# Kernel tuning notes

Hardware: AMD Instinct MI355X
Metric: run time of the kernel (lower is better)

The kernel has to match this reference:

```python
import jax, jax.numpy as jnp
import numpy as np

EMBED_DIM = 1024
NUM_HEADS = 16
HEAD_DIM = EMBED_DIM // NUM_HEADS


def setup_inputs() -> dict:
    key = jax.random.key(0)
    k_h, k_q, k_k, k_v, k_o = jax.random.split(key, 5)
    scale = 1.0 / np.sqrt(EMBED_DIM)
    return {
        "h": jax.random.normal(k_h, (2, 2048, EMBED_DIM), dtype=jnp.float32),
        "W_q": jax.random.normal(k_q, (EMBED_DIM, EMBED_DIM), dtype=jnp.float32) * scale,
        "W_k": jax.random.normal(k_k, (EMBED_DIM, EMBED_DIM), dtype=jnp.float32) * scale,
        "W_v": jax.random.normal(k_v, (EMBED_DIM, EMBED_DIM), dtype=jnp.float32) * scale,
        "W_o": jax.random.normal(k_o, (EMBED_DIM, EMBED_DIM), dtype=jnp.float32) * scale,
    }


def reference(h, W_q, W_k, W_v, W_o):
    B, S, E = h.shape
    H, D = NUM_HEADS, HEAD_DIM
    # nn.Linear stores weight as [out, in]; y = x @ W.T
    q = (h @ W_q.T).reshape(B, S, H, D).transpose(0, 2, 1, 3)  # [B,H,S,D]
    k = (h @ W_k.T).reshape(B, S, H, D).transpose(0, 2, 1, 3)
    v = (h @ W_v.T).reshape(B, S, H, D).transpose(0, 2, 1, 3)
    scores = jnp.einsum("bhsd,bhtd->bhst", q, k) / np.sqrt(D)
    attn = jax.nn.softmax(scores, axis=-1)
    ctx = jnp.einsum("bhst,bhtd->bhsd", attn, v)  # [B,H,S,D]
    ctx = ctx.transpose(0, 2, 1, 3).reshape(B, S, E)
    return ctx @ W_o.T
```

## Files before the change

### kernel.cpp

```cpp
#include <hip/hip_runtime.h>
#include <hip/hip_bf16.h>

#define B_ 2
#define S_ 2048
#define E_ 1024
#define H_ 16
#define D_ 64
#define M_ (B_*S_)

typedef __attribute__((ext_vector_type(8))) short bf16x8;
typedef __attribute__((ext_vector_type(4))) float f32x4;
typedef __attribute__((ext_vector_type(8))) unsigned short u16x8;
typedef __attribute__((ext_vector_type(4))) unsigned short u16x4;

__device__ __forceinline__ unsigned short f2bf_hw(float f) {
  union { __hip_bfloat16 h; unsigned short u; } c;
  c.h = __float2bfloat16(f);
  return c.u;
}

__device__ __forceinline__ void gload_lds16(const void* g, void* l) {
  __builtin_amdgcn_global_load_lds(
      (const __attribute__((address_space(1))) void*)g,
      (__attribute__((address_space(3))) void*)l, 16, 0, 0);
}

__global__ __launch_bounds__(256) void cvt_all(const float* __restrict__ h,
                                               const float* __restrict__ Wq,
                                               const float* __restrict__ Wk,
                                               const float* __restrict__ Wv,
                                               const float* __restrict__ Wo,
                                               unsigned short* __restrict__ dst,
                                               float qscale) {
  int i = blockIdx.x * 256 + threadIdx.x;
  const float4* src4;
  int idx;
  float scale = 1.f;
  if (i < (1 << 20)) {
    src4 = (const float4*)h; idx = i;
  } else {
    int t = i - (1 << 20);
    int j = t >> 18;
    idx = t & ((1 << 18) - 1);
    src4 = (const float4*)((j == 0) ? Wq : (j == 1) ? Wk : (j == 2) ? Wv : Wo);
    if (j == 0) scale = qscale;
  }
  float4 v = src4[idx];
  u16x4 o;
  o[0] = f2bf_hw(v.x * scale);
  o[1] = f2bf_hw(v.y * scale);
  o[2] = f2bf_hw(v.z * scale);
  o[3] = f2bf_hw(v.w * scale);
  ((u16x4*)dst)[i] = o;
}

template<int OUT_BF16>
__device__ __forceinline__ void gemm_body(const unsigned short* __restrict__ A,
                                          const unsigned short* __restrict__ W,
                                          void* __restrict__ Cv,
                                          int row0, int col0, int N, int K,
                                          unsigned short* As, unsigned short* Bs) {
  const int tid = threadIdx.x;
  const int lane = tid & 63, wave = tid >> 6;
  const int wr = wave >> 1, wc = wave & 1;
  const int lq = lane & 15, lg = lane >> 4;
  f32x4 acc[4][4] = {};

  for (int kt = 0; kt < K; kt += 32) {
#pragma unroll
    for (int i = 0; i < 2; ++i) {
      int t = tid + i * 256;
      int rr = t >> 2;
      int sch = (t & 3) ^ ((rr >> 1) & 3);
      gload_lds16(A + (size_t)(row0 + rr) * K + kt + sch * 8, &As[t * 8]);
      gload_lds16(W + (size_t)(col0 + rr) * K + kt + sch * 8, &Bs[t * 8]);
    }
    __syncthreads();
    bf16x8 af[4], bfr[4];
#pragma unroll
    for (int mi = 0; mi < 4; ++mi) {
      int row = wr * 64 + mi * 16 + lq;
      af[mi] = *(const bf16x8*)&As[row * 32 + (lg ^ ((row >> 1) & 3)) * 8];
    }
#pragma unroll
    for (int ni = 0; ni < 4; ++ni) {
      int row = wc * 64 + ni * 16 + lq;
      bfr[ni] = *(const bf16x8*)&Bs[row * 32 + (lg ^ ((row >> 1) & 3)) * 8];
    }
#pragma unroll
    for (int mi = 0; mi < 4; ++mi)
#pragma unroll
      for (int ni = 0; ni < 4; ++ni)
        acc[mi][ni] = __builtin_amdgcn_mfma_f32_16x16x32_bf16(af[mi], bfr[ni], acc[mi][ni], 0, 0, 0);
    __syncthreads();
  }

#pragma unroll
  for (int mi = 0; mi < 4; ++mi)
#pragma unroll
    for (int ni = 0; ni < 4; ++ni) {
      int row = row0 + wr * 64 + mi * 16 + lg * 4;
      int col = col0 + wc * 64 + ni * 16 + lq;
#pragma unroll
      for (int r = 0; r < 4; ++r) {
        float v = acc[mi][ni][r];
        if (OUT_BF16) ((unsigned short*)Cv)[(size_t)(row + r) * N + col] = f2bf_hw(v);
        else          ((float*)Cv)[(size_t)(row + r) * N + col] = v;
      }
    }
}

__global__ __launch_bounds__(256) void gemm_qkv(const unsigned short* __restrict__ A,
                                                const unsigned short* __restrict__ Wq,
                                                const unsigned short* __restrict__ Wk,
                                                const unsigned short* __restrict__ Wv,
                                                unsigned short* __restrict__ Qb,
                                                unsigned short* __restrict__ Kb,
                                                unsigned short* __restrict__ Vb) {
  __shared__ unsigned short As[128 * 32];
  __shared__ unsigned short Bs[128 * 32];
  const int mat = blockIdx.y >> 3;
  const int col0 = (blockIdx.y & 7) * 128;
  const unsigned short* W = (mat == 0) ? Wq : (mat == 1) ? Wk : Wv;
  unsigned short* C = (mat == 0) ? Qb : (mat == 1) ? Kb : Vb;
  gemm_body<1>(A, W, C, blockIdx.x * 128, col0, E_, E_, As, Bs);
}

__global__ __launch_bounds__(256) void gemm_out(const unsigned short* __restrict__ A,
                                                const unsigned short* __restrict__ W,
                                                float* __restrict__ C) {
  __shared__ unsigned short As[128 * 32];
  __shared__ unsigned short Bs[128 * 32];
  gemm_body<0>(A, W, C, blockIdx.x * 128, blockIdx.y * 128, E_, E_, As, Bs);
}

__global__ __launch_bounds__(256) void transpose_v(const unsigned short* __restrict__ V,
                                                   unsigned short* __restrict__ VT) {
  __shared__ unsigned short tile[64][72];
  const int tid = threadIdx.x;
  const int s0 = blockIdx.x * 64;
  const int h = blockIdx.y;
  const int b = blockIdx.z;
  const int r = tid >> 3;
  const int c = (tid & 7) * 8;
  const unsigned short* src = V + ((size_t)(b * S_) + s0) * E_ + h * 64;
#pragma unroll
  for (int i = 0; i < 2; ++i) {
    int rr = r + i * 32;
    u16x8 v = *(const u16x8*)(src + (size_t)rr * E_ + c);
#pragma unroll
    for (int j = 0; j < 8; ++j) tile[rr][c + j] = v[j];
  }
  __syncthreads();
  unsigned short* dst = VT + ((size_t)((b * H_ + h) * 64)) * S_ + s0;
#pragma unroll
  for (int i = 0; i < 2; ++i) {
    int d = r + i * 32;
    u16x8 o;
#pragma unroll
    for (int j = 0; j < 8; ++j) o[j] = tile[c + j][d];
    *(u16x8*)(dst + (size_t)d * S_ + c) = o;
  }
}

__global__ __launch_bounds__(256) void attn(const unsigned short* __restrict__ Q,
                                            const unsigned short* __restrict__ K,
                                            const unsigned short* __restrict__ VT,
                                            unsigned short* __restrict__ ctx) {
  __shared__ unsigned short Ks[2][64 * 64];
  __shared__ unsigned short Vs[2][64 * 64];
  __shared__ unsigned short Ps[4][16 * 72];
  const int tid = threadIdx.x, lane = tid & 63, wave = tid >> 6;
  const int lq = lane & 15, lg = lane >> 4;
  const int bh = blockIdx.y, b = bh >> 4, h = bh & 15;
  const int q0 = blockIdx.x * 64;

  const unsigned short* Qbase = Q + ((size_t)(b * S_) + q0 + wave * 16 + lq) * E_ + h * 64;
  bf16x8 qf0 = *(const bf16x8*)(Qbase + lg * 8);
  bf16x8 qf1 = *(const bf16x8*)(Qbase + 32 + lg * 8);
  const unsigned short* Kbase = K + (size_t)(b * S_) * E_ + h * 64;
  const unsigned short* Vtb = VT + (size_t)((b * H_ + h) * 64) * S_;
  unsigned short* Pw = Ps[wave];

  auto STAGE = [&](int buf, int kc) {
#pragma unroll
    for (int i = 0; i < 2; ++i) {
      int tt = tid + i * 256;
      int r = tt >> 3;
      int sch = (tt & 7) ^ (r & 7);
      gload_lds16(Kbase + (size_t)(kc + r) * E_ + sch * 8, &Ks[buf][tt * 8]);
      gload_lds16(Vtb + (size_t)r * S_ + kc + sch * 8, &Vs[buf][tt * 8]);
    }
  };

  f32x4 oacc[4] = {};
  float m_run = -1e30f, l_run = 0.f;

  STAGE(0, 0);
  asm volatile("s_waitcnt vmcnt(0)" ::: "memory");
  __builtin_amdgcn_s_barrier();

  int cur = 0;
  for (int kc = 0; kc < S_; kc += 64) {
    const bool pref = (kc + 64 < S_);
    if (pref) STAGE(cur ^ 1, kc + 64);

    const unsigned short* Kc = Ks[cur];
    const unsigned short* Vc = Vs[cur];

    f32x4 st[4] = {};
#pragma unroll
    for (int mf = 0; mf < 4; ++mf) {
      int row = mf * 16 + lq;
      bf16x8 kf0 = *(const bf16x8*)&Kc[row * 64 + ((lg ^ (row & 7)) * 8)];
      bf16x8 kf1 = *(const bf16x8*)&Kc[row * 64 + (((4 + lg) ^ (row & 7)) * 8)];
      st[mf] = __builtin_amdgcn_mfma_f32_16x16x32_bf16(kf0, qf0, st[mf], 0, 0, 0);
      st[mf] = __builtin_amdgcn_mfma_f32_16x16x32_bf16(kf1, qf1, st[mf], 0, 0, 0);
    }

    float c0 = fmaxf(fmaxf(st[0][0], st[0][1]), fmaxf(st[0][2], st[0][3]));
    float c1 = fmaxf(fmaxf(st[1][0], st[1][1]), fmaxf(st[1][2], st[1][3]));
    float c2 = fmaxf(fmaxf(st[2][0], st[2][1]), fmaxf(st[2][2], st[2][3]));
    float c3 = fmaxf(fmaxf(st[3][0], st[3][1]), fmaxf(st[3][2], st[3][3]));
    float cm = fmaxf(fmaxf(c0, c1), fmaxf(c2, c3));
    cm = fmaxf(cm, __shfl_xor(cm, 16));
    cm = fmaxf(cm, __shfl_xor(cm, 32));

    if (!__all(cm - m_run <= 8.f)) {
      float m_new = fmaxf(m_run, cm);
      float alpha = __builtin_amdgcn_exp2f(m_run - m_new);
#pragma unroll
      for (int r = 0; r < 4; ++r) {
        float ar = __shfl(alpha, lg * 4 + r);
#pragma unroll
        for (int nf = 0; nf < 4; ++nf) oacc[nf][r] *= ar;
      }
      l_run *= alpha;
      m_run = m_new;
    }

    float ls = 0.f;
#pragma unroll
    for (int mf = 0; mf < 4; ++mf) {
      u16x4 pb;
#pragma unroll
      for (int r = 0; r < 4; ++r) {
        float p = __builtin_amdgcn_exp2f(st[mf][r] - m_run);
        ls += p;
        pb[r] = f2bf_hw(p);
      }
      *(u16x4*)&Pw[lq * 72 + mf * 16 + lg * 4] = pb;
    }
    ls += __shfl_xor(ls, 16);
    ls += __shfl_xor(ls, 32);
    l_run += ls;
    asm volatile("s_waitcnt lgkmcnt(0)" ::: "memory");

#pragma unroll
    for (int ks = 0; ks < 2; ++ks) {
      bf16x8 pf = *(const bf16x8*)&Pw[lq * 72 + ks * 32 + lg * 8];
#pragma unroll
      for (int nf = 0; nf < 4; ++nf) {
        int row = nf * 16 + lq;
        bf16x8 vf = *(const bf16x8*)&Vc[row * 64 + (((ks * 4 + lg) ^ (row & 7)) * 8)];
        oacc[nf] = __builtin_amdgcn_mfma_f32_16x16x32_bf16(pf, vf, oacc[nf], 0, 0, 0);
      }
    }

    if (pref) {
      asm volatile("s_waitcnt vmcnt(0)" ::: "memory");
      __builtin_amdgcn_s_barrier();
      cur ^= 1;
    }
  }

#pragma unroll
  for (int r = 0; r < 4; ++r) {
    float lr = __shfl(l_run, lg * 4 + r);
    float inv = 1.f / lr;
#pragma unroll
    for (int nf = 0; nf < 4; ++nf) {
      ctx[((size_t)(b * S_) + q0 + wave * 16 + lg * 4 + r) * E_ + h * 64 + nf * 16 + lq] =
          f2bf_hw(oacc[nf][r] * inv);
    }
  }
}

extern "C" void kernel_launch(void* const* d_in, const int* in_sizes, int n_in,
                              void* d_out, int out_size, void* d_ws, size_t ws_size,
                              hipStream_t stream) {
  const float* h  = (const float*)d_in[0];
  const float* Wq = (const float*)d_in[1];
  const float* Wk = (const float*)d_in[2];
  const float* Wv = (const float*)d_in[3];
  const float* Wo = (const float*)d_in[4];
  float* out = (float*)d_out;
  char* ws = (char*)d_ws;

  const size_t SZ_H = (size_t)M_ * E_ * 2;
  const size_t SZ_W = (size_t)E_ * E_ * 2;
  unsigned short* hb  = (unsigned short*)(ws);
  unsigned short* wqb = (unsigned short*)(ws + SZ_H);
  unsigned short* wkb = (unsigned short*)(ws + SZ_H + SZ_W);
  unsigned short* wvb = (unsigned short*)(ws + SZ_H + 2 * SZ_W);
  unsigned short* wob = (unsigned short*)(ws + SZ_H + 3 * SZ_W);
  unsigned short* Qb  = (unsigned short*)(ws + SZ_H + 4 * SZ_W);
  unsigned short* Kb  = (unsigned short*)(ws + 2 * SZ_H + 4 * SZ_W);
  unsigned short* Vb  = (unsigned short*)(ws + 3 * SZ_H + 4 * SZ_W);
  unsigned short* VTb = hb;
  unsigned short* Cb  = Vb;

  const float QSCALE = 0.125f * 1.44269504f;
  cvt_all<<<8192, 256, 0, stream>>>(h, Wq, Wk, Wv, Wo, hb, QSCALE);

  gemm_qkv<<<dim3(M_ / 128, 3 * E_ / 128), 256, 0, stream>>>(hb, wqb, wkb, wvb, Qb, Kb, Vb);

  transpose_v<<<dim3(S_ / 64, H_, B_), 256, 0, stream>>>(Vb, VTb);

  attn<<<dim3(S_ / 64, B_ * H_), 256, 0, stream>>>(Qb, Kb, VTb, Cb);

  gemm_out<<<dim3(M_ / 128, E_ / 128), 256, 0, stream>>>(Cb, wob, out);
}
```

Measured before the change: 225.6 us.

## Prefetch K/V tiles through registers into a single LDS buffer with MFMA priority

```diff
diff --git a/kernel.cpp b/kernel.cpp
--- a/kernel.cpp
+++ b/kernel.cpp
@@ -167,8 +167,8 @@
                                             const unsigned short* __restrict__ K,
                                             const unsigned short* __restrict__ VT,
                                             unsigned short* __restrict__ ctx) {
-  __shared__ unsigned short Ks[2][64 * 64];
-  __shared__ unsigned short Vs[2][64 * 64];
+  __shared__ unsigned short Ks[64 * 64];
+  __shared__ unsigned short Vs[64 * 64];
   __shared__ unsigned short Ps[4][16 * 72];
   const int tid = threadIdx.x, lane = tid & 63, wave = tid >> 6;
   const int lq = lane & 15, lg = lane >> 4;
@@ -182,41 +182,45 @@
   const unsigned short* Vtb = VT + (size_t)((b * H_ + h) * 64) * S_;
   unsigned short* Pw = Ps[wave];
 
-  auto STAGE = [&](int buf, int kc) {
-#pragma unroll
-    for (int i = 0; i < 2; ++i) {
-      int tt = tid + i * 256;
-      int r = tt >> 3;
-      int sch = (tt & 7) ^ (r & 7);
-      gload_lds16(Kbase + (size_t)(kc + r) * E_ + sch * 8, &Ks[buf][tt * 8]);
-      gload_lds16(Vtb + (size_t)r * S_ + kc + sch * 8, &Vs[buf][tt * 8]);
-    }
+  const int r0_ = tid >> 3, ch_ = tid & 7;
+  const int r1_ = (tid + 256) >> 3;
+  uint4 kreg[2], vreg[2];
+
+  auto LOADREG = [&](int kc) {
+    kreg[0] = *(const uint4*)(Kbase + (size_t)(kc + r0_) * E_ + ch_ * 8);
+    vreg[0] = *(const uint4*)(Vtb + (size_t)r0_ * S_ + kc + ch_ * 8);
+    kreg[1] = *(const uint4*)(Kbase + (size_t)(kc + r1_) * E_ + ch_ * 8);
+    vreg[1] = *(const uint4*)(Vtb + (size_t)r1_ * S_ + kc + ch_ * 8);
+  };
+  auto WRITELDS = [&]() {
+    *(uint4*)&Ks[(r0_ * 8 + (ch_ ^ (r0_ & 7))) * 8] = kreg[0];
+    *(uint4*)&Vs[(r0_ * 8 + (ch_ ^ (r0_ & 7))) * 8] = vreg[0];
+    *(uint4*)&Ks[(r1_ * 8 + (ch_ ^ (r1_ & 7))) * 8] = kreg[1];
+    *(uint4*)&Vs[(r1_ * 8 + (ch_ ^ (r1_ & 7))) * 8] = vreg[1];
   };
 
   f32x4 oacc[4] = {};
   float m_run = -1e30f, l_run = 0.f;
 
-  STAGE(0, 0);
-  asm volatile("s_waitcnt vmcnt(0)" ::: "memory");
-  __builtin_amdgcn_s_barrier();
-
-  int cur = 0;
+  LOADREG(0);
+  WRITELDS();
+  __syncthreads();
+
   for (int kc = 0; kc < S_; kc += 64) {
     const bool pref = (kc + 64 < S_);
-    if (pref) STAGE(cur ^ 1, kc + 64);
-
-    const unsigned short* Kc = Ks[cur];
-    const unsigned short* Vc = Vs[cur];
+    if (pref) LOADREG(kc + 64);
 
     f32x4 st[4] = {};
+    __builtin_amdgcn_s_setprio(1);
 #pragma unroll
     for (int mf = 0; mf < 4; ++mf) {
       int row = mf * 16 + lq;
-      bf16x8 kf0 = *(const bf16x8*)&Kc[row * 64 + ((lg ^ (row & 7)) * 8)];
-      bf16x8 kf1 = *(const bf16x8*)&Kc[row * 64 + (((4 + lg) ^ (row & 7)) * 8)];
+      bf16x8 kf0 = *(const bf16x8*)&Ks[row * 64 + ((lg ^ (row & 7)) * 8)];
+      bf16x8 kf1 = *(const bf16x8*)&Ks[row * 64 + (((4 + lg) ^ (row & 7)) * 8)];
       st[mf] = __builtin_amdgcn_mfma_f32_16x16x32_bf16(kf0, qf0, st[mf], 0, 0, 0);
       st[mf] = __builtin_amdgcn_mfma_f32_16x16x32_bf16(kf1, qf1, st[mf], 0, 0, 0);
     }
+    __builtin_amdgcn_s_setprio(0);
 
     float c0 = fmaxf(fmaxf(st[0][0], st[0][1]), fmaxf(st[0][2], st[0][3]));
     float c1 = fmaxf(fmaxf(st[1][0], st[1][1]), fmaxf(st[1][2], st[1][3]));
@@ -256,21 +260,23 @@
     l_run += ls;
     asm volatile("s_waitcnt lgkmcnt(0)" ::: "memory");
 
+    __builtin_amdgcn_s_setprio(1);
 #pragma unroll
     for (int ks = 0; ks < 2; ++ks) {
       bf16x8 pf = *(const bf16x8*)&Pw[lq * 72 + ks * 32 + lg * 8];
 #pragma unroll
       for (int nf = 0; nf < 4; ++nf) {
         int row = nf * 16 + lq;
-        bf16x8 vf = *(const bf16x8*)&Vc[row * 64 + (((ks * 4 + lg) ^ (row & 7)) * 8)];
+        bf16x8 vf = *(const bf16x8*)&Vs[row * 64 + (((ks * 4 + lg) ^ (row & 7)) * 8)];
         oacc[nf] = __builtin_amdgcn_mfma_f32_16x16x32_bf16(pf, vf, oacc[nf], 0, 0, 0);
       }
     }
+    __builtin_amdgcn_s_setprio(0);
 
     if (pref) {
-      asm volatile("s_waitcnt vmcnt(0)" ::: "memory");
-      __builtin_amdgcn_s_barrier();
-      cur ^= 1;
+      __syncthreads();
+      WRITELDS();
+      __syncthreads();
     }
   }
 
```

Result: slower. 290.3 us (+28.7%).
